# Optimization experiments

Measured on AMD Instinct MI355X. Metric: run time of the kernel, lower is better.

The kernel has to match this reference:

```python
import jax, jax.numpy as jnp
import numpy as np


def setup_inputs() -> dict:
    key = jax.random.key(0)
    k0, k1, k2, k3 = jax.random.split(key, 4)
    T, H, I, E, K = 2048, 2048, 1408, 8, 2  # tokens, hidden, intermediate, experts, top-k
    hidden_states = jax.random.normal(k0, (T, H), dtype=jnp.float32)
    router_weight = jax.random.normal(k1, (H, E), dtype=jnp.float32) * 0.02
    gate_up_weight = jax.random.normal(k2, (E, H, 2 * I), dtype=jnp.float32) * 0.02
    down_weight = jax.random.normal(k3, (E, I, H), dtype=jnp.float32) * 0.02
    return {
        "hidden_states": hidden_states,
        "router_weight": router_weight,
        "gate_up_weight": gate_up_weight,
        "down_weight": down_weight,
        "top_k": K,
    }


def reference(hidden_states, router_weight, gate_up_weight, down_weight, top_k):
    # Router: logits -> softmax -> top-k -> renormalize ('normalization' path)
    router_logits = hidden_states @ router_weight                  # [T, E]
    router_weights = jax.nn.softmax(router_logits, axis=-1)       # [T, E]
    topk_w, topk_idx = jax.lax.top_k(router_weights, top_k)       # [T, K]
    topk_w = topk_w / jnp.sum(topk_w, axis=-1, keepdims=True)     # router_weights_topk_reduced

    T, H = hidden_states.shape
    I = down_weight.shape[1]

    # Grouped gate_up GEMM (dense-per-expert reference for the grouped GMM)
    gate_up = jnp.einsum('th,ehf->etf', hidden_states, gate_up_weight)  # [E, T, 2I]
    gate, up = gate_up[..., :I], gate_up[..., I:]
    swish_out = jax.nn.silu(gate) * up                              # SWIGLU  [E, T, I]
    mlp_out = jnp.einsum('eti,eih->eth', swish_out, down_weight)    # [E, T, H]

    # Scatter-combine: gather each token's top-k expert outputs, weighted sum
    sel = mlp_out[topk_idx, jnp.arange(T)[:, None]]                 # [T, K, H]
    out = jnp.sum(sel * topk_w[..., None], axis=1)                  # [T, H]
    return out
```

## Files before the change

kernel.cpp:

```cpp
#include <hip/hip_runtime.h>
#include <hip/hip_bf16.h>
#include <math.h>

#define T_TOK 2048
#define HDIM  2048
#define IDIM  1408
#define NG    2816
#define NEXP  8
#define NPAIR (T_TOK*2)
#define RPAD  4160

typedef __attribute__((ext_vector_type(4))) float  f32x4;
typedef __attribute__((ext_vector_type(4))) short  s16x4;
typedef __attribute__((ext_vector_type(8))) short  s16x8;
typedef __attribute__((ext_vector_type(8))) __bf16 bf16x8;

__device__ __forceinline__ short f2bf(float f) {
  union { float f; unsigned u; } v; v.f = f;
  unsigned r = v.u + 0x7FFFu + ((v.u >> 16) & 1u);
  return (short)(r >> 16);
}

__device__ __forceinline__ void gload_lds16(const void* g, void* l) {
  __builtin_amdgcn_global_load_lds((const __attribute__((address_space(1))) unsigned int*)g,
                                   (__attribute__((address_space(3))) unsigned int*)l,
                                   16, 0, 0);
}

__global__ void router_kernel(const float* __restrict__ hs, const float* __restrict__ rw,
                              int* __restrict__ pair_e, float* __restrict__ pair_w,
                              int* __restrict__ pair_pos, int* __restrict__ counts) {
  int wid = threadIdx.x >> 6, lane = threadIdx.x & 63;
  int t = blockIdx.x * 4 + wid;
  float acc[NEXP];
#pragma unroll
  for (int e = 0; e < NEXP; e++) acc[e] = 0.f;
  const float* h = hs + (size_t)t * HDIM;
  for (int k = lane; k < HDIM; k += 64) {
    float x = h[k];
    f32x4 w0 = *(const f32x4*)(rw + (size_t)k * NEXP);
    f32x4 w1 = *(const f32x4*)(rw + (size_t)k * NEXP + 4);
#pragma unroll
    for (int e = 0; e < 4; e++) { acc[e] += x * w0[e]; acc[e + 4] += x * w1[e]; }
  }
#pragma unroll
  for (int e = 0; e < NEXP; e++)
#pragma unroll
    for (int off = 32; off > 0; off >>= 1)
      acc[e] += __shfl_xor(acc[e], off, 64);
  if (lane == 0) {
    int i1 = 0; float v1 = acc[0];
#pragma unroll
    for (int e = 1; e < NEXP; e++) if (acc[e] > v1) { v1 = acc[e]; i1 = e; }
    int i2 = -1; float v2 = -3.4e38f;
#pragma unroll
    for (int e = 0; e < NEXP; e++) if (e != i1 && acc[e] > v2) { v2 = acc[e]; i2 = e; }
    float w2 = 1.f / (1.f + expf(v1 - v2));
    float w1 = 1.f - w2;
    int p1 = atomicAdd(&counts[i1], 1);
    int p2 = atomicAdd(&counts[i2], 1);
    pair_e[2*t]   = i1; pair_w[2*t]   = w1; pair_pos[2*t]   = p1;
    pair_e[2*t+1] = i2; pair_w[2*t+1] = w2; pair_pos[2*t+1] = p2;
  }
}

__global__ void prefix_kernel(const int* __restrict__ counts, int* __restrict__ offs) {
  if (threadIdx.x == 0) {
    int s = 0;
    for (int e = 0; e < NEXP; e++) { offs[e] = s; s += (counts[e] + 7) & ~7; }
    offs[NEXP] = s;
  }
}

__global__ void rowmap_kernel(const int* __restrict__ pair_e, const float* __restrict__ pair_w,
                              const int* __restrict__ pair_pos, const int* __restrict__ offs,
                              int* __restrict__ row_token, float* __restrict__ row_weight) {
  int p = blockIdx.x * 256 + threadIdx.x;
  if (p >= NPAIR) return;
  int e = pair_e[p];
  int row = offs[e] + pair_pos[p];
  row_token[row] = p >> 1;
  row_weight[row] = pair_w[p];
}

__global__ __launch_bounds__(256) void gather_kernel(const float* __restrict__ hs,
                                                     const int* __restrict__ row_token,
                                                     short* __restrict__ A_c) {
  int r = blockIdx.x;
  int tok = row_token[r];
  if (tok < 0) return;
  int t = threadIdx.x;
  const float* src = hs + (size_t)tok * HDIM + t * 8;
  f32x4 v0 = *(const f32x4*)src;
  f32x4 v1 = *(const f32x4*)(src + 4);
  s16x8 o;
#pragma unroll
  for (int j = 0; j < 4; j++) { o[j] = f2bf(v0[j]); o[4 + j] = f2bf(v1[j]); }
  int dstg = (t & ~7) | ((t & 7) ^ (r & 7));
  *(s16x8*)&A_c[(size_t)r * HDIM + dstg * 8] = o;
}

__global__ __launch_bounds__(256) void convert_w_kernel(
    const float* __restrict__ src, short* __restrict__ dst, int K, int N, int e_base) {
  int e = blockIdx.z + e_base;
  src += (size_t)e * K * N;
  dst += (size_t)blockIdx.z * K * N;
  int n0 = blockIdx.x * 64, k0 = blockIdx.y * 64;
  __shared__ short tile[64 * 76];
  int tid = threadIdx.x;
#pragma unroll
  for (int it = 0; it < 4; it++) {
    int s = tid + it * 256;
    int kk = s >> 4, nn = (s & 15) * 4;
    f32x4 v = *(const f32x4*)(src + (size_t)(k0 + kk) * N + n0 + nn);
    s16x4 b;
#pragma unroll
    for (int j = 0; j < 4; j++) b[j] = f2bf(v[j]);
    *(s16x4*)&tile[kk * 76 + nn] = b;
  }
  __syncthreads();
#pragma unroll
  for (int it = 0; it < 2; it++) {
    int s = tid + it * 256;
    int n = s >> 3, g = s & 7;
    int gs = g ^ (n & 7);
    s16x8 o;
#pragma unroll
    for (int j = 0; j < 8; j++) o[j] = tile[(gs * 8 + j) * 76 + n];
    *(s16x8*)&dst[(size_t)(n0 + n) * K + k0 + g * 8] = o;
  }
}

__global__ __launch_bounds__(256) void gateup_kernel(
    const short* __restrict__ A_c, const short* __restrict__ W,
    const int* __restrict__ counts, const int* __restrict__ offs,
    short* __restrict__ S, int e_base, size_t w_e_stride) {
  int e = blockIdx.z + e_base;
  int cnt = counts[e];
  int rb = blockIdx.y * 128;
  if (rb >= cnt) return;
  int nb = blockIdx.x;
  int row0 = offs[e] + rb;
  const short* Ar = A_c + (size_t)row0 * HDIM;
  const short* Wb = W + (size_t)blockIdx.z * w_e_stride;
  const short* Bg = Wb + (size_t)(nb * 64) * HDIM;
  const short* Bu = Wb + (size_t)(IDIM + nb * 64) * HDIM;
  __shared__ short As[128 * 64];
  __shared__ short Bgs[64 * 64];
  __shared__ short Bus[64 * 64];
  int tid = threadIdx.x, lane = tid & 63, wid = tid >> 6;
  int wm = wid >> 1, wn = wid & 1;
  int lm = lane & 15, lg = lane >> 4;
  f32x4 accg[4][2], accu[4][2];
#pragma unroll
  for (int a = 0; a < 4; a++)
#pragma unroll
    for (int b = 0; b < 2; b++) { accg[a][b] = (f32x4)0.f; accu[a][b] = (f32x4)0.f; }

  for (int kt = 0; kt < HDIM / 64; kt++) {
    int k0 = kt * 64;
    __syncthreads();
#pragma unroll
    for (int it = 0; it < 4; it++) {
      int idx = tid + it * 256;
      gload_lds16(Ar + (size_t)(idx >> 3) * HDIM + k0 + (idx & 7) * 8, &As[idx * 8]);
    }
#pragma unroll
    for (int it = 0; it < 2; it++) {
      int idx = tid + it * 256;
      gload_lds16(Bg + (size_t)(idx >> 3) * HDIM + k0 + (idx & 7) * 8, &Bgs[idx * 8]);
      gload_lds16(Bu + (size_t)(idx >> 3) * HDIM + k0 + (idx & 7) * 8, &Bus[idx * 8]);
    }
    __syncthreads();
#pragma unroll
    for (int ks = 0; ks < 2; ks++) {
      bf16x8 a[4], bg[2], bu[2];
#pragma unroll
      for (int mi = 0; mi < 4; mi++) {
        int m = wm * 64 + mi * 16 + lm;
        a[mi] = *(const bf16x8*)&As[m * 64 + (((ks * 4 + lg) ^ (m & 7)) * 8)];
      }
#pragma unroll
      for (int nf = 0; nf < 2; nf++) {
        int n = wn * 32 + nf * 16 + lm;
        int off = n * 64 + (((ks * 4 + lg) ^ (n & 7)) * 8);
        bg[nf] = *(const bf16x8*)&Bgs[off];
        bu[nf] = *(const bf16x8*)&Bus[off];
      }
#pragma unroll
      for (int mi = 0; mi < 4; mi++)
#pragma unroll
        for (int nf = 0; nf < 2; nf++) {
          accg[mi][nf] = __builtin_amdgcn_mfma_f32_16x16x32_bf16(a[mi], bg[nf], accg[mi][nf], 0, 0, 0);
          accu[mi][nf] = __builtin_amdgcn_mfma_f32_16x16x32_bf16(a[mi], bu[nf], accu[mi][nf], 0, 0, 0);
        }
    }
  }
#pragma unroll
  for (int mi = 0; mi < 4; mi++)
#pragma unroll
    for (int nf = 0; nf < 2; nf++)
#pragma unroll
      for (int j = 0; j < 4; j++) {
        int row = wm * 64 + mi * 16 + lg * 4 + j;
        if (rb + row < cnt) {
          int rg = row0 + row;
          int c6 = wn * 32 + nf * 16 + lm;
          int dc = (((c6 >> 3) ^ (rg & 7)) << 3) | (c6 & 7);
          float g = accg[mi][nf][j], u = accu[mi][nf][j];
          float sv = (g / (1.f + expf(-g))) * u;
          S[(size_t)rg * IDIM + nb * 64 + dc] = f2bf(sv);
        }
      }
}

__global__ __launch_bounds__(256) void down_kernel(
    const short* __restrict__ S, const short* __restrict__ W,
    const int* __restrict__ counts, const int* __restrict__ offs,
    const int* __restrict__ row_token, const float* __restrict__ row_weight,
    float* __restrict__ out, int e_base, size_t w_e_stride) {
  int e = blockIdx.z + e_base;
  int cnt = counts[e];
  int rb = blockIdx.y * 128;
  if (rb >= cnt) return;
  int nb = blockIdx.x;
  int row0 = offs[e] + rb;
  const short* Ar = S + (size_t)row0 * IDIM;
  const short* Bw = W + (size_t)blockIdx.z * w_e_stride + (size_t)(nb * 128) * IDIM;
  __shared__ short As[128 * 64];
  __shared__ short Bs[128 * 64];
  int tid = threadIdx.x, lane = tid & 63, wid = tid >> 6;
  int wm = wid >> 1, wn = wid & 1;
  int lm = lane & 15, lg = lane >> 4;
  f32x4 acc[4][4];
#pragma unroll
  for (int a = 0; a < 4; a++)
#pragma unroll
    for (int b = 0; b < 4; b++) acc[a][b] = (f32x4)0.f;

  for (int kt = 0; kt < IDIM / 64; kt++) {
    int k0 = kt * 64;
    __syncthreads();
#pragma unroll
    for (int it = 0; it < 4; it++) {
      int idx = tid + it * 256;
      gload_lds16(Ar + (size_t)(idx >> 3) * IDIM + k0 + (idx & 7) * 8, &As[idx * 8]);
      gload_lds16(Bw + (size_t)(idx >> 3) * IDIM + k0 + (idx & 7) * 8, &Bs[idx * 8]);
    }
    __syncthreads();
#pragma unroll
    for (int ks = 0; ks < 2; ks++) {
      bf16x8 a[4], b[4];
#pragma unroll
      for (int mi = 0; mi < 4; mi++) {
        int m = wm * 64 + mi * 16 + lm;
        a[mi] = *(const bf16x8*)&As[m * 64 + (((ks * 4 + lg) ^ (m & 7)) * 8)];
      }
#pragma unroll
      for (int nf = 0; nf < 4; nf++) {
        int n = wn * 64 + nf * 16 + lm;
        b[nf] = *(const bf16x8*)&Bs[n * 64 + (((ks * 4 + lg) ^ (n & 7)) * 8)];
      }
#pragma unroll
      for (int mi = 0; mi < 4; mi++)
#pragma unroll
        for (int nf = 0; nf < 4; nf++)
          acc[mi][nf] = __builtin_amdgcn_mfma_f32_16x16x32_bf16(a[mi], b[nf], acc[mi][nf], 0, 0, 0);
    }
  }
#pragma unroll
  for (int mi = 0; mi < 4; mi++)
#pragma unroll
    for (int j = 0; j < 4; j++) {
      int row = wm * 64 + mi * 16 + lg * 4 + j;
      if (rb + row < cnt) {
        int tok = row_token[row0 + row];
        float w = row_weight[row0 + row];
#pragma unroll
        for (int nf = 0; nf < 4; nf++) {
          int col = nb * 128 + wn * 64 + nf * 16 + lm;
          atomicAdd(&out[(size_t)tok * HDIM + col], acc[mi][nf][j] * w);
        }
      }
    }
}

extern "C" void kernel_launch(void* const* d_in, const int* in_sizes, int n_in,
                              void* d_out, int out_size, void* d_ws, size_t ws_size,
                              hipStream_t stream) {
  const float* hs  = (const float*)d_in[0];
  const float* rw  = (const float*)d_in[1];
  const float* guw = (const float*)d_in[2];
  const float* dw  = (const float*)d_in[3];
  float* out = (float*)d_out;

  char* ws = (char*)d_ws;
  size_t off = 0;
  auto take = [&](size_t b) { size_t p = off; off = (off + b + 255) & ~(size_t)255; return p; };
  size_t s_off   = take((size_t)RPAD * IDIM * 2);
  int*   counts     = (int*)(ws + take(32 * 4));
  int*   offs       = (int*)(ws + take(16 * 4));
  int*   pair_e     = (int*)(ws + take(NPAIR * 4));
  float* pair_w     = (float*)(ws + take(NPAIR * 4));
  int*   pair_pos   = (int*)(ws + take(NPAIR * 4));
  int*   row_token  = (int*)(ws + take(RPAD * 4));
  float* row_weight = (float*)(ws + take(RPAD * 4));
  size_t ac_off  = take((size_t)RPAD * HDIM * 2);
  size_t wg_off  = off;

  short* S   = (short*)(ws + s_off);
  short* A_c = (short*)(ws + ac_off);

  const size_t WG_BYTES = (size_t)NEXP * NG * HDIM * 2;
  const size_t WSLOT    = (size_t)NG * HDIM * 2;
  bool full = ws_size >= wg_off + WG_BYTES;

  hipMemsetAsync(counts, 0, 32 * 4, stream);
  hipMemsetAsync(row_token, 0xFF, RPAD * 4, stream);
  hipMemsetAsync(d_out, 0, (size_t)T_TOK * HDIM * 4, stream);

  router_kernel<<<T_TOK / 4, 256, 0, stream>>>(hs, rw, pair_e, pair_w, pair_pos, counts);
  prefix_kernel<<<1, 64, 0, stream>>>(counts, offs);
  rowmap_kernel<<<NPAIR / 256, 256, 0, stream>>>(pair_e, pair_w, pair_pos, offs,
                                                 row_token, row_weight);
  gather_kernel<<<RPAD, 256, 0, stream>>>(hs, row_token, A_c);

  if (full) {
    short* Wg = (short*)(ws + wg_off);
    short* Wd = (short*)(ws + ac_off);
    convert_w_kernel<<<dim3(NG / 64, HDIM / 64, NEXP), 256, 0, stream>>>(guw, Wg, HDIM, NG, 0);
    gateup_kernel<<<dim3(IDIM / 64, T_TOK / 128, NEXP), 256, 0, stream>>>(
        A_c, Wg, counts, offs, S, 0, (size_t)NG * HDIM);
    convert_w_kernel<<<dim3(HDIM / 64, IDIM / 64, NEXP), 256, 0, stream>>>(dw, Wd, IDIM, HDIM, 0);
    down_kernel<<<dim3(HDIM / 128, T_TOK / 128, NEXP), 256, 0, stream>>>(
        S, Wd, counts, offs, row_token, row_weight, out, 0, (size_t)HDIM * IDIM);
  } else {
    short* slot = (short*)(ws + wg_off);
    (void)WSLOT;
    for (int e = 0; e < NEXP; e++) {
      convert_w_kernel<<<dim3(NG / 64, HDIM / 64, 1), 256, 0, stream>>>(guw, slot, HDIM, NG, e);
      gateup_kernel<<<dim3(IDIM / 64, T_TOK / 128, 1), 256, 0, stream>>>(
          A_c, slot, counts, offs, S, e, 0);
    }
    for (int e = 0; e < NEXP; e++) {
      convert_w_kernel<<<dim3(HDIM / 64, IDIM / 64, 1), 256, 0, stream>>>(dw, slot, IDIM, HDIM, e);
      down_kernel<<<dim3(HDIM / 128, T_TOK / 128, 1), 256, 0, stream>>>(
          S, slot, counts, offs, row_token, row_weight, out, e, 0);
    }
  }
}
```

Measured before the change: 333.1 us.

## Double-buffer LDS in expert GEMMs and use compact per-block grid with XCD remap

The gate_up and down GEMMs now double-buffer their LDS tiles, so the next k-tile's global-to-LDS loads are issued before the current tile's MFMAs and only one barrier is needed per iteration. Each expert's row segment is padded to a multiple of 128 and the launch uses a flat grid of 40 row blocks. Each block finds its expert from the offsets, which removes the many empty blocks of the old 3D per-expert grid. A remap spreads consecutive workgroups across the 8 XCDs for L2 locality, and padding rows are zero-filled so bounds checks can go. In exchange the kernels use twice the LDS and the workspace and padded compute grow.

```diff
diff --git a/kernel.cpp b/kernel.cpp
--- a/kernel.cpp
+++ b/kernel.cpp
@@ -8,7 +8,7 @@
 #define NG    2816
 #define NEXP  8
 #define NPAIR (T_TOK*2)
-#define RPAD  4160
+#define RPAD  5120
 
 typedef __attribute__((ext_vector_type(4))) float  f32x4;
 typedef __attribute__((ext_vector_type(4))) short  s16x4;
@@ -25,6 +25,14 @@
   __builtin_amdgcn_global_load_lds((const __attribute__((address_space(1))) unsigned int*)g,
                                    (__attribute__((address_space(3))) unsigned int*)l,
                                    16, 0, 0);
+}
+
+__device__ __forceinline__ void grid_remap(int orig, int NB, int* nb, int* rblk) {
+  int wgid = (orig & 7) * (NB * 5) + (orig >> 3);
+  int cid = wgid / (NB * 5), c = wgid % (NB * 5);
+  int nbg = c / 10, rem = c % 10;
+  *rblk = (rem >> 1) * 8 + cid;
+  *nb = nbg * 2 + (rem & 1);
 }
 
 __global__ void router_kernel(const float* __restrict__ hs, const float* __restrict__ rw,
@@ -67,7 +75,7 @@
 __global__ void prefix_kernel(const int* __restrict__ counts, int* __restrict__ offs) {
   if (threadIdx.x == 0) {
     int s = 0;
-    for (int e = 0; e < NEXP; e++) { offs[e] = s; s += (counts[e] + 7) & ~7; }
+    for (int e = 0; e < NEXP; e++) { offs[e] = s; s += (counts[e] + 127) & ~127; }
     offs[NEXP] = s;
   }
 }
@@ -88,8 +96,11 @@
                                                      short* __restrict__ A_c) {
   int r = blockIdx.x;
   int tok = row_token[r];
-  if (tok < 0) return;
   int t = threadIdx.x;
+  if (tok < 0) {
+    *(s16x8*)&A_c[(size_t)r * HDIM + t * 8] = (s16x8)0;
+    return;
+  }
   const float* src = hs + (size_t)tok * HDIM + t * 8;
   f32x4 v0 = *(const f32x4*)src;
   f32x4 v1 = *(const f32x4*)(src + 4);
@@ -133,59 +144,71 @@
 
 __global__ __launch_bounds__(256) void gateup_kernel(
     const short* __restrict__ A_c, const short* __restrict__ W,
-    const int* __restrict__ counts, const int* __restrict__ offs,
-    short* __restrict__ S, int e_base, size_t w_e_stride) {
-  int e = blockIdx.z + e_base;
-  int cnt = counts[e];
-  int rb = blockIdx.y * 128;
-  if (rb >= cnt) return;
-  int nb = blockIdx.x;
-  int row0 = offs[e] + rb;
-  const short* Ar = A_c + (size_t)row0 * HDIM;
-  const short* Wb = W + (size_t)blockIdx.z * w_e_stride;
+    const int* __restrict__ offs, short* __restrict__ S,
+    int e_only, size_t w_e_stride) {
+  int orig = blockIdx.y * gridDim.x + blockIdx.x;
+  int nb, rblk;
+  grid_remap(orig, 22, &nb, &rblk);
+  int rb = rblk * 128;
+  if (rb >= offs[NEXP]) return;
+  int e = 0;
+#pragma unroll
+  for (int i = 1; i < NEXP; i++) e += (rb >= offs[i]);
+  if (e_only >= 0 && e != e_only) return;
+  const short* Wb = W + (e_only >= 0 ? 0 : (size_t)e * w_e_stride);
+  const short* Ar = A_c + (size_t)rb * HDIM;
   const short* Bg = Wb + (size_t)(nb * 64) * HDIM;
   const short* Bu = Wb + (size_t)(IDIM + nb * 64) * HDIM;
-  __shared__ short As[128 * 64];
-  __shared__ short Bgs[64 * 64];
-  __shared__ short Bus[64 * 64];
+
+  __shared__ short As[2][128 * 64];
+  __shared__ short Bgs[2][64 * 64];
+  __shared__ short Bus[2][64 * 64];
   int tid = threadIdx.x, lane = tid & 63, wid = tid >> 6;
   int wm = wid >> 1, wn = wid & 1;
   int lm = lane & 15, lg = lane >> 4;
+
   f32x4 accg[4][2], accu[4][2];
 #pragma unroll
   for (int a = 0; a < 4; a++)
 #pragma unroll
     for (int b = 0; b < 2; b++) { accg[a][b] = (f32x4)0.f; accu[a][b] = (f32x4)0.f; }
 
-  for (int kt = 0; kt < HDIM / 64; kt++) {
+  auto STAGE = [&](int buf, int kt) {
     int k0 = kt * 64;
-    __syncthreads();
 #pragma unroll
     for (int it = 0; it < 4; it++) {
       int idx = tid + it * 256;
-      gload_lds16(Ar + (size_t)(idx >> 3) * HDIM + k0 + (idx & 7) * 8, &As[idx * 8]);
+      gload_lds16(Ar + (size_t)(idx >> 3) * HDIM + k0 + (idx & 7) * 8, &As[buf][idx * 8]);
     }
 #pragma unroll
     for (int it = 0; it < 2; it++) {
       int idx = tid + it * 256;
-      gload_lds16(Bg + (size_t)(idx >> 3) * HDIM + k0 + (idx & 7) * 8, &Bgs[idx * 8]);
-      gload_lds16(Bu + (size_t)(idx >> 3) * HDIM + k0 + (idx & 7) * 8, &Bus[idx * 8]);
-    }
-    __syncthreads();
+      gload_lds16(Bg + (size_t)(idx >> 3) * HDIM + k0 + (idx & 7) * 8, &Bgs[buf][idx * 8]);
+      gload_lds16(Bu + (size_t)(idx >> 3) * HDIM + k0 + (idx & 7) * 8, &Bus[buf][idx * 8]);
+    }
+  };
+
+  STAGE(0, 0);
+  asm volatile("s_waitcnt vmcnt(0)" ::: "memory");
+  __builtin_amdgcn_s_barrier();
+  int cur = 0;
+  for (int kt = 0; kt < HDIM / 64; kt++) {
+    if (kt + 1 < HDIM / 64) STAGE(cur ^ 1, kt + 1);
+    asm volatile("" ::: "memory");
 #pragma unroll
     for (int ks = 0; ks < 2; ks++) {
       bf16x8 a[4], bg[2], bu[2];
 #pragma unroll
       for (int mi = 0; mi < 4; mi++) {
         int m = wm * 64 + mi * 16 + lm;
-        a[mi] = *(const bf16x8*)&As[m * 64 + (((ks * 4 + lg) ^ (m & 7)) * 8)];
+        a[mi] = *(const bf16x8*)&As[cur][m * 64 + (((ks * 4 + lg) ^ (m & 7)) * 8)];
       }
 #pragma unroll
       for (int nf = 0; nf < 2; nf++) {
         int n = wn * 32 + nf * 16 + lm;
         int off = n * 64 + (((ks * 4 + lg) ^ (n & 7)) * 8);
-        bg[nf] = *(const bf16x8*)&Bgs[off];
-        bu[nf] = *(const bf16x8*)&Bus[off];
+        bg[nf] = *(const bf16x8*)&Bgs[cur][off];
+        bu[nf] = *(const bf16x8*)&Bus[cur][off];
       }
 #pragma unroll
       for (int mi = 0; mi < 4; mi++)
@@ -195,6 +218,9 @@
           accu[mi][nf] = __builtin_amdgcn_mfma_f32_16x16x32_bf16(a[mi], bu[nf], accu[mi][nf], 0, 0, 0);
         }
     }
+    asm volatile("s_waitcnt vmcnt(0)" ::: "memory");
+    __builtin_amdgcn_s_barrier();
+    cur ^= 1;
   }
 #pragma unroll
   for (int mi = 0; mi < 4; mi++)
@@ -203,63 +229,73 @@
 #pragma unroll
       for (int j = 0; j < 4; j++) {
         int row = wm * 64 + mi * 16 + lg * 4 + j;
-        if (rb + row < cnt) {
-          int rg = row0 + row;
-          int c6 = wn * 32 + nf * 16 + lm;
-          int dc = (((c6 >> 3) ^ (rg & 7)) << 3) | (c6 & 7);
-          float g = accg[mi][nf][j], u = accu[mi][nf][j];
-          float sv = (g / (1.f + expf(-g))) * u;
-          S[(size_t)rg * IDIM + nb * 64 + dc] = f2bf(sv);
-        }
+        int rg = rb + row;
+        int c6 = wn * 32 + nf * 16 + lm;
+        int dc = (((c6 >> 3) ^ (rg & 7)) << 3) | (c6 & 7);
+        float g = accg[mi][nf][j], u = accu[mi][nf][j];
+        float sv = (g / (1.f + expf(-g))) * u;
+        S[(size_t)rg * IDIM + nb * 64 + dc] = f2bf(sv);
       }
 }
 
 __global__ __launch_bounds__(256) void down_kernel(
     const short* __restrict__ S, const short* __restrict__ W,
-    const int* __restrict__ counts, const int* __restrict__ offs,
-    const int* __restrict__ row_token, const float* __restrict__ row_weight,
-    float* __restrict__ out, int e_base, size_t w_e_stride) {
-  int e = blockIdx.z + e_base;
-  int cnt = counts[e];
-  int rb = blockIdx.y * 128;
-  if (rb >= cnt) return;
-  int nb = blockIdx.x;
-  int row0 = offs[e] + rb;
-  const short* Ar = S + (size_t)row0 * IDIM;
-  const short* Bw = W + (size_t)blockIdx.z * w_e_stride + (size_t)(nb * 128) * IDIM;
-  __shared__ short As[128 * 64];
-  __shared__ short Bs[128 * 64];
+    const int* __restrict__ offs, const int* __restrict__ row_token,
+    const float* __restrict__ row_weight, float* __restrict__ out,
+    int e_only, size_t w_e_stride) {
+  int orig = blockIdx.y * gridDim.x + blockIdx.x;
+  int nb, rblk;
+  grid_remap(orig, 16, &nb, &rblk);
+  int rb = rblk * 128;
+  if (rb >= offs[NEXP]) return;
+  int e = 0;
+#pragma unroll
+  for (int i = 1; i < NEXP; i++) e += (rb >= offs[i]);
+  if (e_only >= 0 && e != e_only) return;
+  const short* Ar = S + (size_t)rb * IDIM;
+  const short* Bw = W + (e_only >= 0 ? 0 : (size_t)e * w_e_stride) + (size_t)(nb * 128) * IDIM;
+
+  __shared__ short As[2][128 * 64];
+  __shared__ short Bs[2][128 * 64];
   int tid = threadIdx.x, lane = tid & 63, wid = tid >> 6;
   int wm = wid >> 1, wn = wid & 1;
   int lm = lane & 15, lg = lane >> 4;
+
   f32x4 acc[4][4];
 #pragma unroll
   for (int a = 0; a < 4; a++)
 #pragma unroll
     for (int b = 0; b < 4; b++) acc[a][b] = (f32x4)0.f;
 
-  for (int kt = 0; kt < IDIM / 64; kt++) {
+  auto STAGE = [&](int buf, int kt) {
     int k0 = kt * 64;
-    __syncthreads();
 #pragma unroll
     for (int it = 0; it < 4; it++) {
       int idx = tid + it * 256;
-      gload_lds16(Ar + (size_t)(idx >> 3) * IDIM + k0 + (idx & 7) * 8, &As[idx * 8]);
-      gload_lds16(Bw + (size_t)(idx >> 3) * IDIM + k0 + (idx & 7) * 8, &Bs[idx * 8]);
-    }
-    __syncthreads();
+      gload_lds16(Ar + (size_t)(idx >> 3) * IDIM + k0 + (idx & 7) * 8, &As[buf][idx * 8]);
+      gload_lds16(Bw + (size_t)(idx >> 3) * IDIM + k0 + (idx & 7) * 8, &Bs[buf][idx * 8]);
+    }
+  };
+
+  STAGE(0, 0);
+  asm volatile("s_waitcnt vmcnt(0)" ::: "memory");
+  __builtin_amdgcn_s_barrier();
+  int cur = 0;
+  for (int kt = 0; kt < IDIM / 64; kt++) {
+    if (kt + 1 < IDIM / 64) STAGE(cur ^ 1, kt + 1);
+    asm volatile("" ::: "memory");
 #pragma unroll
     for (int ks = 0; ks < 2; ks++) {
       bf16x8 a[4], b[4];
 #pragma unroll
       for (int mi = 0; mi < 4; mi++) {
         int m = wm * 64 + mi * 16 + lm;
-        a[mi] = *(const bf16x8*)&As[m * 64 + (((ks * 4 + lg) ^ (m & 7)) * 8)];
+        a[mi] = *(const bf16x8*)&As[cur][m * 64 + (((ks * 4 + lg) ^ (m & 7)) * 8)];
       }
 #pragma unroll
       for (int nf = 0; nf < 4; nf++) {
         int n = wn * 64 + nf * 16 + lm;
-        b[nf] = *(const bf16x8*)&Bs[n * 64 + (((ks * 4 + lg) ^ (n & 7)) * 8)];
+        b[nf] = *(const bf16x8*)&Bs[cur][n * 64 + (((ks * 4 + lg) ^ (n & 7)) * 8)];
       }
 #pragma unroll
       for (int mi = 0; mi < 4; mi++)
@@ -267,15 +303,18 @@
         for (int nf = 0; nf < 4; nf++)
           acc[mi][nf] = __builtin_amdgcn_mfma_f32_16x16x32_bf16(a[mi], b[nf], acc[mi][nf], 0, 0, 0);
     }
+    asm volatile("s_waitcnt vmcnt(0)" ::: "memory");
+    __builtin_amdgcn_s_barrier();
+    cur ^= 1;
   }
 #pragma unroll
   for (int mi = 0; mi < 4; mi++)
 #pragma unroll
     for (int j = 0; j < 4; j++) {
       int row = wm * 64 + mi * 16 + lg * 4 + j;
-      if (rb + row < cnt) {
-        int tok = row_token[row0 + row];
-        float w = row_weight[row0 + row];
+      int tok = row_token[rb + row];
+      if (tok >= 0) {
+        float w = row_weight[rb + row];
 #pragma unroll
         for (int nf = 0; nf < 4; nf++) {
           int col = nb * 128 + wn * 64 + nf * 16 + lm;
@@ -297,7 +336,7 @@
   char* ws = (char*)d_ws;
   size_t off = 0;
   auto take = [&](size_t b) { size_t p = off; off = (off + b + 255) & ~(size_t)255; return p; };
-  size_t s_off   = take((size_t)RPAD * IDIM * 2);
+  size_t s_off      = take((size_t)RPAD * IDIM * 2);
   int*   counts     = (int*)(ws + take(32 * 4));
   int*   offs       = (int*)(ws + take(16 * 4));
   int*   pair_e     = (int*)(ws + take(NPAIR * 4));
@@ -312,7 +351,6 @@
   short* A_c = (short*)(ws + ac_off);
 
   const size_t WG_BYTES = (size_t)NEXP * NG * HDIM * 2;
-  const size_t WSLOT    = (size_t)NG * HDIM * 2;
   bool full = ws_size >= wg_off + WG_BYTES;
 
   hipMemsetAsync(counts, 0, 32 * 4, stream);
@@ -329,23 +367,19 @@
     short* Wg = (short*)(ws + wg_off);
     short* Wd = (short*)(ws + ac_off);
     convert_w_kernel<<<dim3(NG / 64, HDIM / 64, NEXP), 256, 0, stream>>>(guw, Wg, HDIM, NG, 0);
-    gateup_kernel<<<dim3(IDIM / 64, T_TOK / 128, NEXP), 256, 0, stream>>>(
-        A_c, Wg, counts, offs, S, 0, (size_t)NG * HDIM);
+    gateup_kernel<<<dim3(22, 40, 1), 256, 0, stream>>>(A_c, Wg, offs, S, -1, (size_t)NG * HDIM);
     convert_w_kernel<<<dim3(HDIM / 64, IDIM / 64, NEXP), 256, 0, stream>>>(dw, Wd, IDIM, HDIM, 0);
-    down_kernel<<<dim3(HDIM / 128, T_TOK / 128, NEXP), 256, 0, stream>>>(
-        S, Wd, counts, offs, row_token, row_weight, out, 0, (size_t)HDIM * IDIM);
+    down_kernel<<<dim3(16, 40, 1), 256, 0, stream>>>(S, Wd, offs, row_token, row_weight, out,
+                                                     -1, (size_t)HDIM * IDIM);
   } else {
     short* slot = (short*)(ws + wg_off);
-    (void)WSLOT;
     for (int e = 0; e < NEXP; e++) {
       convert_w_kernel<<<dim3(NG / 64, HDIM / 64, 1), 256, 0, stream>>>(guw, slot, HDIM, NG, e);
-      gateup_kernel<<<dim3(IDIM / 64, T_TOK / 128, 1), 256, 0, stream>>>(
-          A_c, slot, counts, offs, S, e, 0);
+      gateup_kernel<<<dim3(22, 40, 1), 256, 0, stream>>>(A_c, slot, offs, S, e, 0);
     }
     for (int e = 0; e < NEXP; e++) {
       convert_w_kernel<<<dim3(HDIM / 64, IDIM / 64, 1), 256, 0, stream>>>(dw, slot, IDIM, HDIM, e);
-      down_kernel<<<dim3(HDIM / 128, T_TOK / 128, 1), 256, 0, stream>>>(
-          S, slot, counts, offs, row_token, row_weight, out, e, 0);
-    }
-  }
-}
+      down_kernel<<<dim3(16, 40, 1), 256, 0, stream>>>(S, slot, offs, row_token, row_weight, out, e, 0);
+    }
+  }
+}
```

After: 336.2 us. No clear change (+0.9%).
